# Kernel optimization log

Measured on AMD Instinct MI355X. Metric: run time of the kernel, lower is better.

Reference implementation:

```python
import jax, jax.numpy as jnp
import numpy as np

N_NODES = 50000
N_EDGES = 800000
F_IN = 64
HID = 256
EMB = 128
N_LAYERS = 3


def setup_inputs() -> dict:
    key = jax.random.key(0)
    ks = jax.random.split(key, 20)
    s = lambda i, shape: jax.random.normal(ks[i], shape, dtype=jnp.float32) * 0.05
    inp = {
        'x': jax.random.normal(ks[0], (N_NODES, F_IN), dtype=jnp.float32),
        'edge_index': jax.random.randint(ks[1], (2, N_EDGES), 0, N_NODES, dtype=jnp.int64),
        # node_encoder: Linear(F_IN,HID) -> ReLU -> Dropout -> Linear(HID,HID)
        'W1': s(2, (F_IN, HID)), 'b1': s(3, (HID,)),
        'W2': s(4, (HID, HID)), 'b2': s(5, (HID,)),
        # stacked GCN layer weights [L,HID,HID], biases [L,HID]
        'conv_W': s(6, (N_LAYERS, HID, HID)), 'conv_b': s(7, (N_LAYERS, HID)),
        # graph_projection: Linear(2H,H) -> ReLU -> Dropout -> Linear(H,EMB)
        'Wg1': s(8, (2 * HID, HID)), 'bg1': s(9, (HID,)),
        'Wg2': s(10, (HID, EMB)), 'bg2': s(11, (EMB,)),
        # decoder node_projection: Linear(EMB,H) -> ReLU -> Linear(H,H)
        'Wd1': s(12, (EMB, HID)), 'bd1': s(13, (HID,)),
        'Wd2': s(14, (HID, HID)), 'bd2': s(15, (HID,)),
    }
    return inp


def _forward(x, edge_index, W1, b1, W2, b2, conv_W, conv_b, Wg1, bg1, Wg2, bg2, Wd1, bd1, Wd2, bd2):
    N = x.shape[0]
    # node encoder (dropout is identity in eval)
    h = jax.nn.relu(x @ W1 + b1) @ W2 + b2  # [N,H]

    # GCN normalization with self-loops (PyG GCNConv defaults)
    self_idx = jnp.arange(N, dtype=edge_index.dtype)
    src = jnp.concatenate([edge_index[0], self_idx])  # [E+N]
    dst = jnp.concatenate([edge_index[1], self_idx])
    deg = jax.ops.segment_sum(jnp.ones_like(dst, dtype=h.dtype), dst, num_segments=N)
    dinv = jnp.where(deg > 0, jax.lax.rsqrt(deg), 0.0)
    norm = (dinv[src] * dinv[dst])[:, None]  # [E+N,1]

    for l in range(N_LAYERS):
        hw = h @ conv_W[l]                              # [N,H]
        msg = hw[src] * norm                            # gather + scale
        h = jax.ops.segment_sum(msg, dst, num_segments=N) + conv_b[l]
        h = jax.nn.relu(h)

    # global mean + max pool (single graph)
    graph_rep = jnp.concatenate([h.mean(axis=0), h.max(axis=0)])[None, :]  # [1,2H]
    graph_embedding = jax.nn.relu(graph_rep @ Wg1 + bg1) @ Wg2 + bg2       # [1,EMB]

    # decoder: project graph embedding, broadcast to all nodes, score edges
    v = jax.nn.relu(graph_embedding @ Wd1 + bd1) @ Wd2 + bd2  # [1,H]
    node_emb = jnp.broadcast_to(v, (N, v.shape[1]))           # [N,H]
    row, col = edge_index[0], edge_index[1]
    edge_logits = jnp.sum(node_emb[row] * node_emb[col], axis=1)  # [E]
    edge_probs = jax.nn.sigmoid(edge_logits)
    return graph_embedding, edge_probs


def reference(x, edge_index, W1, b1, W2, b2, conv_W, conv_b, Wg1, bg1, Wg2, bg2, Wd1, bd1, Wd2, bd2):
    return _forward(x, edge_index, W1, b1, W2, b2, conv_W, conv_b, Wg1, bg1, Wg2, bg2, Wd1, bd1, Wd2, bd2)
```

## Files before the change

### kernel.cpp

```cpp
#include <hip/hip_runtime.h>
#include <hip/hip_bf16.h>


typedef __attribute__((ext_vector_type(8))) short bf16x8;
typedef __attribute__((ext_vector_type(4))) float f32x4;
typedef __attribute__((ext_vector_type(2))) float f32x2;

#define FP8_SCALE 32.0f
#define FP8_INV (1.0f / 32.0f)

__device__ __forceinline__ ushort f2bf(float f) {
  union { float f; unsigned u; } v; v.f = f;
  unsigned r = v.u + 0x7FFF + ((v.u >> 16) & 1);
  return (ushort)(r >> 16);
}
__device__ __forceinline__ float bf2f(ushort b) {
  union { unsigned u; float f; } v; v.u = ((unsigned)b) << 16;
  return v.f;
}


__global__ void init_detect_kernel(const int* __restrict__ ei, int* __restrict__ flag,
                                   int* __restrict__ cnt8, int N8) {
  int i = blockIdx.x * 256 + threadIdx.x;
  if (i < N8) cnt8[i] = 0;
  if (blockIdx.x == 0 && threadIdx.x == 0) {
    int all0 = 1;
    for (int k = 0; k < 128; ++k) {
      if (ei[2 * k + 1] != 0) { all0 = 0; break; }
    }
    flag[0] = all0;
  }
}

__global__ void count_kernel(const int* __restrict__ ei, const int* __restrict__ flag,
                             int* __restrict__ cnt8, int* __restrict__ rank,
                             unsigned* __restrict__ pairs, int E, int N) {
  int e = blockIdx.x * 256 + threadIdx.x;
  if (e >= E) return;
  int s, d;
  if (flag[0]) {
    const long long* e64 = (const long long*)ei;
    s = (int)e64[e];
    d = (int)e64[(size_t)E + e];
  } else {
    s = ei[e];
    d = ei[(size_t)E + e];
  }
  rank[e] = atomicAdd(&cnt8[(size_t)(blockIdx.x & 7) * N + d], 1);
  pairs[e] = (unsigned)s | ((unsigned)d << 16);
}


__global__ __launch_bounds__(256) void bsum_kernel(const int* __restrict__ cnt8,
                                                   int* __restrict__ cnt,
                                                   int* __restrict__ bsum, int N) {
  __shared__ int red[4];
  int t = threadIdx.x;
  int i = blockIdx.x * 256 + t;
  int v = 0;
  if (i < N) {
#pragma unroll
    for (int c = 0; c < 8; ++c) v += cnt8[(size_t)c * N + i];
    cnt[i] = v;
  }
  for (int off = 32; off > 0; off >>= 1) v += __shfl_down(v, off, 64);
  if ((t & 63) == 0) red[t >> 6] = v;
  __syncthreads();
  if (t == 0) bsum[blockIdx.x] = red[0] + red[1] + red[2] + red[3];
}

__global__ __launch_bounds__(256) void bscan_kernel(const int* __restrict__ bsum,
                                                    int* __restrict__ boff,
                                                    int* __restrict__ rowptr, int B, int N) {
  __shared__ int s[256];
  int t = threadIdx.x;
  int v = (t < B) ? bsum[t] : 0;
  s[t] = v;
  __syncthreads();
  for (int off = 1; off < 256; off <<= 1) {
    int x = s[t];
    int add = (t >= off) ? s[t - off] : 0;
    __syncthreads();
    s[t] = x + add;
    __syncthreads();
  }
  if (t < B) boff[t] = s[t] - v;
  if (t == 255) rowptr[N] = s[255];
}

__global__ __launch_bounds__(256) void rowptr_kernel(const int* __restrict__ cnt,
                                                     const int* __restrict__ cnt8,
                                                     const int* __restrict__ boff,
                                                     int* __restrict__ rowptr,
                                                     int* __restrict__ base8,
                                                     float* __restrict__ dinv, int N) {
  __shared__ int s[256];
  int t = threadIdx.x;
  int i = blockIdx.x * 256 + t;
  int v = (i < N) ? cnt[i] : 0;
  s[t] = v;
  __syncthreads();
  for (int off = 1; off < 256; off <<= 1) {
    int x = s[t];
    int add = (t >= off) ? s[t - off] : 0;
    __syncthreads();
    s[t] = x + add;
    __syncthreads();
  }
  if (i < N) {
    int rp = boff[blockIdx.x] + s[t] - v;
    rowptr[i] = rp;
    int run = rp;
#pragma unroll
    for (int c = 0; c < 8; ++c) {
      base8[(size_t)c * N + i] = run;
      run += cnt8[(size_t)c * N + i];
    }
    dinv[i] = rsqrtf((float)(v + 1));
  }
}


__global__ void scatter_pack_kernel(const unsigned* __restrict__ pairs,
                                    const int* __restrict__ rank,
                                    const int* __restrict__ base8,
                                    ushort* __restrict__ col, int E, int N, int nScat,
                                    const float* __restrict__ W1, ushort* __restrict__ Wp1,
                                    const float* __restrict__ W2, ushort* __restrict__ Wp2,
                                    const float* __restrict__ cW, ushort* __restrict__ Wpc) {
  int b = blockIdx.x;
  if (b < nScat) {
    int e = b * 256 + threadIdx.x;
    if (e >= E) return;
    unsigned p = pairs[e];
    int s = p & 0xffff;
    int d = p >> 16;
    int c = (e >> 8) & 7;
    int pos = base8[(size_t)c * N + d] + rank[e];
    col[pos] = (ushort)s;
    return;
  }
  b -= nScat;
  const float* W;
  ushort* Wp;
  int K;
  if (b < 8) { W = W1; Wp = Wp1; K = 64; }
  else if (b < 40) { W = W2; Wp = Wp2; K = 256; b -= 8; }
  else {
    int l = (b - 40) >> 5;
    W = cW + (size_t)l * 256 * 256;
    Wp = Wpc + (size_t)l * 8 * 16 * 64 * 8;
    K = 256;
    b -= 40 + l * 32;
  }
  int idx = b * 256 + threadIdx.x;
  int total = (K >> 5) * 16 * 64;
  if (idx >= total) return;
  int lane = idx & 63;
  int cb = (idx >> 6) & 15;
  int ks = idx >> 10;
  int nn = cb * 16 + (lane & 15);
  int kbase = ks * 32 + (lane >> 4) * 8;
#pragma unroll
  for (int i = 0; i < 8; ++i)
    Wp[(size_t)idx * 8 + i] = f2bf(W[(size_t)(kbase + i) * 256 + nn]);
}


template <int NKS, bool AF32>
__global__ __launch_bounds__(256) void gemm_mfma_kernel(
    const void* __restrict__ Av,
    const ushort* __restrict__ Wp,
    const float* __restrict__ bias,
    const float* __restrict__ scale,
    ushort* __restrict__ C,
    unsigned char* __restrict__ C8,
    int M, int relu) {
  constexpr int K = NKS * 32;
  int t = threadIdx.x;
  int lane = t & 63, wave = t >> 6;
  int l15 = lane & 15, lk = lane >> 4;
  int row0 = blockIdx.x * 64;

  f32x4 acc[4][4];
#pragma unroll
  for (int rb = 0; rb < 4; ++rb)
#pragma unroll
    for (int cb = 0; cb < 4; ++cb) acc[rb][cb] = (f32x4){0.f, 0.f, 0.f, 0.f};

  const ushort* abase[4];
  const float* afbase[4];
#pragma unroll
  for (int rb = 0; rb < 4; ++rb) {
    int arow = row0 + rb * 16 + l15;
    if (AF32) arow = min(arow, M - 1);
    if (AF32) afbase[rb] = (const float*)Av + (size_t)arow * K + lk * 8;
    else      abase[rb] = (const ushort*)Av + (size_t)arow * K + lk * 8;
  }
  const ushort* bbase = Wp + ((size_t)(wave * 4) * 64 + lane) * 8;

#pragma unroll
  for (int ks = 0; ks < NKS; ++ks) {
    bf16x8 a[4], b[4];
#pragma unroll
    for (int rb = 0; rb < 4; ++rb) {
      if (AF32) {
        float4 f0 = *reinterpret_cast<const float4*>(afbase[rb] + ks * 32);
        float4 f1 = *reinterpret_cast<const float4*>(afbase[rb] + ks * 32 + 4);
        bf16x8 av;
        av[0] = (short)f2bf(f0.x); av[1] = (short)f2bf(f0.y);
        av[2] = (short)f2bf(f0.z); av[3] = (short)f2bf(f0.w);
        av[4] = (short)f2bf(f1.x); av[5] = (short)f2bf(f1.y);
        av[6] = (short)f2bf(f1.z); av[7] = (short)f2bf(f1.w);
        a[rb] = av;
      } else {
        a[rb] = *reinterpret_cast<const bf16x8*>(abase[rb] + ks * 32);
      }
    }
#pragma unroll
    for (int cb = 0; cb < 4; ++cb)
      b[cb] = *reinterpret_cast<const bf16x8*>(bbase + ((size_t)ks * 16 + cb) * 64 * 8);
#pragma unroll
    for (int rb = 0; rb < 4; ++rb)
#pragma unroll
      for (int cb = 0; cb < 4; ++cb)
        acc[rb][cb] = __builtin_amdgcn_mfma_f32_16x16x32_bf16(a[rb], b[cb], acc[rb][cb], 0, 0, 0);
  }

  float bv[4];
#pragma unroll
  for (int cb = 0; cb < 4; ++cb)
    bv[cb] = bias ? bias[wave * 64 + cb * 16 + l15] : 0.f;

#pragma unroll
  for (int rb = 0; rb < 4; ++rb) {
    int rbase = row0 + rb * 16 + lk * 4;
#pragma unroll
    for (int r = 0; r < 4; ++r) {
      int row = rbase + r;
      if (row >= M) continue;
      float sc = scale ? scale[row] : 1.f;
#pragma unroll
      for (int cb = 0; cb < 4; ++cb) {
        float v = acc[rb][cb][r] + bv[cb];
        if (relu) v = fmaxf(v, 0.f);
        v *= sc;
        int colIdx = wave * 64 + cb * 16 + l15;
        if (C8) {
          float vq = fminf(fmaxf(v * FP8_SCALE, -448.f), 448.f);
          unsigned p = __builtin_amdgcn_cvt_pk_fp8_f32(vq, vq, 0, false);
          C8[(size_t)row * 256 + colIdx] = (unsigned char)(p & 0xff);
        } else {
          C[(size_t)row * 256 + colIdx] = f2bf(v);
        }
      }
    }
  }
}


__global__ __launch_bounds__(64) void mp_kernel(const unsigned char* __restrict__ hw8,
                                                const int* __restrict__ rowptr,
                                                const ushort* __restrict__ col,
                                                const float* __restrict__ dinv,
                                                const float* __restrict__ bias,
                                                ushort* __restrict__ hout) {
  int n = blockIdx.x;
  int t = threadIdx.x;
  const unsigned* hw32 = reinterpret_cast<const unsigned*>(hw8);
  unsigned ws = hw32[(size_t)n * 64 + t];
  f32x2 lo = __builtin_amdgcn_cvt_pk_f32_fp8(ws, false);
  f32x2 hi = __builtin_amdgcn_cvt_pk_f32_fp8(ws, true);
  float ax = lo[0], ay = lo[1], az = hi[0], aw = hi[1];
  int beg = rowptr[n], end = rowptr[n + 1];
  int j = beg;
  for (; j + 16 <= end; j += 16) {
    int ss[16];
    unsigned ww[16];
#pragma unroll
    for (int q = 0; q < 16; ++q) ss[q] = col[j + q];
#pragma unroll
    for (int q = 0; q < 16; ++q) ww[q] = hw32[(size_t)ss[q] * 64 + t];
#pragma unroll
    for (int q = 0; q < 16; ++q) {
      f32x2 lq = __builtin_amdgcn_cvt_pk_f32_fp8(ww[q], false);
      f32x2 hq = __builtin_amdgcn_cvt_pk_f32_fp8(ww[q], true);
      ax += lq[0]; ay += lq[1]; az += hq[0]; aw += hq[1];
    }
  }
  for (; j + 4 <= end; j += 4) {
    int s0 = col[j], s1 = col[j + 1], s2 = col[j + 2], s3 = col[j + 3];
    unsigned w0 = hw32[(size_t)s0 * 64 + t];
    unsigned w1 = hw32[(size_t)s1 * 64 + t];
    unsigned w2 = hw32[(size_t)s2 * 64 + t];
    unsigned w3 = hw32[(size_t)s3 * 64 + t];
    f32x2 l0 = __builtin_amdgcn_cvt_pk_f32_fp8(w0, false);
    f32x2 h0 = __builtin_amdgcn_cvt_pk_f32_fp8(w0, true);
    f32x2 l1 = __builtin_amdgcn_cvt_pk_f32_fp8(w1, false);
    f32x2 h1 = __builtin_amdgcn_cvt_pk_f32_fp8(w1, true);
    f32x2 l2 = __builtin_amdgcn_cvt_pk_f32_fp8(w2, false);
    f32x2 h2 = __builtin_amdgcn_cvt_pk_f32_fp8(w2, true);
    f32x2 l3 = __builtin_amdgcn_cvt_pk_f32_fp8(w3, false);
    f32x2 h3 = __builtin_amdgcn_cvt_pk_f32_fp8(w3, true);
    ax += (l0[0] + l1[0]) + (l2[0] + l3[0]);
    ay += (l0[1] + l1[1]) + (l2[1] + l3[1]);
    az += (h0[0] + h1[0]) + (h2[0] + h3[0]);
    aw += (h0[1] + h1[1]) + (h2[1] + h3[1]);
  }
  for (; j < end; ++j) {
    int s = col[j];
    unsigned wv = hw32[(size_t)s * 64 + t];
    f32x2 l2 = __builtin_amdgcn_cvt_pk_f32_fp8(wv, false);
    f32x2 h2 = __builtin_amdgcn_cvt_pk_f32_fp8(wv, true);
    ax += l2[0]; ay += l2[1]; az += h2[0]; aw += h2[1];
  }
  float dn = dinv[n] * FP8_INV;
  float4 bv = *reinterpret_cast<const float4*>(bias + t * 4);
  ushort4 o;
  o.x = f2bf(fmaxf(fmaf(dn, ax, bv.x), 0.f));
  o.y = f2bf(fmaxf(fmaf(dn, ay, bv.y), 0.f));
  o.z = f2bf(fmaxf(fmaf(dn, az, bv.z), 0.f));
  o.w = f2bf(fmaxf(fmaf(dn, aw, bv.w), 0.f));
  *reinterpret_cast<ushort4*>(hout + (size_t)n * 256 + t * 4) = o;
}


__global__ __launch_bounds__(256) void pool_partial_kernel(const ushort* __restrict__ h,
                                                           float* __restrict__ psum,
                                                           float* __restrict__ pmax, int N) {
  __shared__ float ssum[4][256];
  __shared__ float smax[4][256];
  int t = threadIdx.x;
  int w = t >> 6, l = t & 63;
  int gw = blockIdx.x * 4 + w;
  float s0 = 0.f, s1 = 0.f, s2 = 0.f, s3 = 0.f;
  float m0 = 0.f, m1 = 0.f, m2 = 0.f, m3 = 0.f;
  const ushort4 z = {0, 0, 0, 0};
  for (int r = gw; r < N; r += 8192) {
    ushort4 v[8];
#pragma unroll
    for (int j = 0; j < 8; ++j) {
      int rj = r + j * 1024;
      v[j] = (rj < N) ? *reinterpret_cast<const ushort4*>(h + (size_t)rj * 256 + l * 4) : z;
    }
#pragma unroll
    for (int j = 0; j < 8; ++j) {
      float a0 = bf2f(v[j].x), a1 = bf2f(v[j].y), a2 = bf2f(v[j].z), a3 = bf2f(v[j].w);
      s0 += a0; s1 += a1; s2 += a2; s3 += a3;
      m0 = fmaxf(m0, a0); m1 = fmaxf(m1, a1); m2 = fmaxf(m2, a2); m3 = fmaxf(m3, a3);
    }
  }
  ssum[w][l * 4] = s0; ssum[w][l * 4 + 1] = s1; ssum[w][l * 4 + 2] = s2; ssum[w][l * 4 + 3] = s3;
  smax[w][l * 4] = m0; smax[w][l * 4 + 1] = m1; smax[w][l * 4 + 2] = m2; smax[w][l * 4 + 3] = m3;
  __syncthreads();
  float s = ssum[0][t] + ssum[1][t] + ssum[2][t] + ssum[3][t];
  float m = fmaxf(fmaxf(smax[0][t], smax[1][t]), fmaxf(smax[2][t], smax[3][t]));
  psum[(size_t)blockIdx.x * 256 + t] = s;
  pmax[(size_t)blockIdx.x * 256 + t] = m;
}


__global__ __launch_bounds__(1024) void head_kernel(const float* __restrict__ psum,
                                                    const float* __restrict__ pmax,
                                                    const float* __restrict__ Wg1, const float* __restrict__ bg1,
                                                    const float* __restrict__ Wg2, const float* __restrict__ bg2,
                                                    const float* __restrict__ Wd1, const float* __restrict__ bd1,
                                                    const float* __restrict__ Wd2, const float* __restrict__ bd2,
                                                    float* __restrict__ out_ge, float* __restrict__ s_out, int N) {
  __shared__ float gr[512];
  __shared__ float part[4][256];
  __shared__ float t1[256];
  __shared__ float ge[128];
  __shared__ float t2[256];
  __shared__ float vv[256];
  __shared__ float red[4];
  int t = threadIdx.x;
  float* pf = &part[0][0];

  {
    int kg = t >> 8, c = t & 255;
    const float* base = psum + (size_t)(kg * 64) * 256 + c;
    float a = 0.f;
#pragma unroll
    for (int i = 0; i < 64; i += 4)
      a += (base[(size_t)i * 256] + base[(size_t)(i + 1) * 256]) +
           (base[(size_t)(i + 2) * 256] + base[(size_t)(i + 3) * 256]);
    part[kg][c] = a;
  }
  __syncthreads();
  if (t < 256) gr[t] = (part[0][t] + part[1][t] + part[2][t] + part[3][t]) / (float)N;
  __syncthreads();
  {
    int kg = t >> 8, c = t & 255;
    const float* base = pmax + (size_t)(kg * 64) * 256 + c;
    float m = 0.f;
#pragma unroll
    for (int i = 0; i < 64; i += 4)
      m = fmaxf(m, fmaxf(fmaxf(base[(size_t)i * 256], base[(size_t)(i + 1) * 256]),
                         fmaxf(base[(size_t)(i + 2) * 256], base[(size_t)(i + 3) * 256])));
    part[kg][c] = m;
  }
  __syncthreads();
  if (t < 256)
    gr[256 + t] = fmaxf(fmaxf(part[0][t], part[1][t]), fmaxf(part[2][t], part[3][t]));
  __syncthreads();

  {
    int kg = t >> 8, c = t & 255, k0 = kg * 128;
    float a0 = 0, a1 = 0, a2 = 0, a3 = 0, a4 = 0, a5 = 0, a6 = 0, a7 = 0;
    for (int k = k0; k < k0 + 128; k += 8) {
      a0 = fmaf(gr[k + 0], Wg1[(size_t)(k + 0) * 256 + c], a0);
      a1 = fmaf(gr[k + 1], Wg1[(size_t)(k + 1) * 256 + c], a1);
      a2 = fmaf(gr[k + 2], Wg1[(size_t)(k + 2) * 256 + c], a2);
      a3 = fmaf(gr[k + 3], Wg1[(size_t)(k + 3) * 256 + c], a3);
      a4 = fmaf(gr[k + 4], Wg1[(size_t)(k + 4) * 256 + c], a4);
      a5 = fmaf(gr[k + 5], Wg1[(size_t)(k + 5) * 256 + c], a5);
      a6 = fmaf(gr[k + 6], Wg1[(size_t)(k + 6) * 256 + c], a6);
      a7 = fmaf(gr[k + 7], Wg1[(size_t)(k + 7) * 256 + c], a7);
    }
    part[kg][c] = ((a0 + a1) + (a2 + a3)) + ((a4 + a5) + (a6 + a7));
  }
  __syncthreads();
  if (t < 256) t1[t] = fmaxf(part[0][t] + part[1][t] + part[2][t] + part[3][t] + bg1[t], 0.f);
  __syncthreads();

  {
    int kg = t >> 7, c = t & 127, k0 = kg * 32;
    float a0 = 0, a1 = 0, a2 = 0, a3 = 0;
    for (int k = k0; k < k0 + 32; k += 4) {
      a0 = fmaf(t1[k + 0], Wg2[(size_t)(k + 0) * 128 + c], a0);
      a1 = fmaf(t1[k + 1], Wg2[(size_t)(k + 1) * 128 + c], a1);
      a2 = fmaf(t1[k + 2], Wg2[(size_t)(k + 2) * 128 + c], a2);
      a3 = fmaf(t1[k + 3], Wg2[(size_t)(k + 3) * 128 + c], a3);
    }
    pf[kg * 128 + c] = (a0 + a1) + (a2 + a3);
  }
  __syncthreads();
  if (t < 128) {
    float s = bg2[t];
#pragma unroll
    for (int g = 0; g < 8; ++g) s += pf[g * 128 + t];
    ge[t] = s;
    out_ge[t] = s;
  }
  __syncthreads();

  {
    int kg = t >> 8, c = t & 255, k0 = kg * 32;
    float a0 = 0, a1 = 0, a2 = 0, a3 = 0;
    for (int k = k0; k < k0 + 32; k += 4) {
      a0 = fmaf(ge[k + 0], Wd1[(size_t)(k + 0) * 256 + c], a0);
      a1 = fmaf(ge[k + 1], Wd1[(size_t)(k + 1) * 256 + c], a1);
      a2 = fmaf(ge[k + 2], Wd1[(size_t)(k + 2) * 256 + c], a2);
      a3 = fmaf(ge[k + 3], Wd1[(size_t)(k + 3) * 256 + c], a3);
    }
    part[kg][c] = (a0 + a1) + (a2 + a3);
  }
  __syncthreads();
  if (t < 256) t2[t] = fmaxf(part[0][t] + part[1][t] + part[2][t] + part[3][t] + bd1[t], 0.f);
  __syncthreads();

  {
    int kg = t >> 8, c = t & 255, k0 = kg * 64;
    float a0 = 0, a1 = 0, a2 = 0, a3 = 0, a4 = 0, a5 = 0, a6 = 0, a7 = 0;
    for (int k = k0; k < k0 + 64; k += 8) {
      a0 = fmaf(t2[k + 0], Wd2[(size_t)(k + 0) * 256 + c], a0);
      a1 = fmaf(t2[k + 1], Wd2[(size_t)(k + 1) * 256 + c], a1);
      a2 = fmaf(t2[k + 2], Wd2[(size_t)(k + 2) * 256 + c], a2);
      a3 = fmaf(t2[k + 3], Wd2[(size_t)(k + 3) * 256 + c], a3);
      a4 = fmaf(t2[k + 4], Wd2[(size_t)(k + 4) * 256 + c], a4);
      a5 = fmaf(t2[k + 5], Wd2[(size_t)(k + 5) * 256 + c], a5);
      a6 = fmaf(t2[k + 6], Wd2[(size_t)(k + 6) * 256 + c], a6);
      a7 = fmaf(t2[k + 7], Wd2[(size_t)(k + 7) * 256 + c], a7);
    }
    part[kg][c] = ((a0 + a1) + (a2 + a3)) + ((a4 + a5) + (a6 + a7));
  }
  __syncthreads();
  if (t < 256) vv[t] = part[0][t] + part[1][t] + part[2][t] + part[3][t] + bd2[t];
  __syncthreads();

  if (t < 256) {
    float p = vv[t] * vv[t];
    for (int off = 32; off > 0; off >>= 1) p += __shfl_down(p, off, 64);
    if ((t & 63) == 0) red[t >> 6] = p;
  }
  __syncthreads();
  if (t == 0) {
    float ssq = red[0] + red[1] + red[2] + red[3];
    s_out[0] = 1.f / (1.f + expf(-ssq));
  }
}

__global__ void fill_kernel(float* __restrict__ out, const float* __restrict__ s_out, int E) {
  int i = (blockIdx.x * 256 + threadIdx.x) * 4;
  if (i + 4 <= E) {
    float s = s_out[0];
    *reinterpret_cast<float4*>(out + i) = make_float4(s, s, s, s);
  } else {
    for (int j = i; j < E; ++j) out[j] = s_out[0];
  }
}


extern "C" void kernel_launch(void* const* d_in, const int* in_sizes, int n_in,
                              void* d_out, int out_size, void* d_ws, size_t ws_size,
                              hipStream_t stream) {
  const float* x   = (const float*)d_in[0];
  const int*   ei  = (const int*)d_in[1];
  const float* W1  = (const float*)d_in[2];
  const float* b1  = (const float*)d_in[3];
  const float* W2  = (const float*)d_in[4];
  const float* b2  = (const float*)d_in[5];
  const float* cW  = (const float*)d_in[6];
  const float* cb  = (const float*)d_in[7];
  const float* Wg1 = (const float*)d_in[8];
  const float* bg1 = (const float*)d_in[9];
  const float* Wg2 = (const float*)d_in[10];
  const float* bg2 = (const float*)d_in[11];
  const float* Wd1 = (const float*)d_in[12];
  const float* bd1 = (const float*)d_in[13];
  const float* Wd2 = (const float*)d_in[14];
  const float* bd2 = (const float*)d_in[15];
  float* out = (float*)d_out;

  int N = in_sizes[0] / 64;
  int E = in_sizes[1] / 2;
  int Mpad = (N + 63) & ~63;
  int B = (N + 255) / 256;

  size_t off = 0;
  auto walloc = [&](size_t bytes) -> void* {
    void* p = (char*)d_ws + off;
    off += (bytes + 511) & ~(size_t)511;
    return p;
  };
  ushort* hA    = (ushort*)walloc((size_t)Mpad * 256 * 2);
  ushort* hB    = (ushort*)walloc((size_t)Mpad * 256 * 2);
  unsigned char* hA8 = (unsigned char*)walloc((size_t)Mpad * 256);
  ushort* Wp1   = (ushort*)walloc((size_t)2 * 16 * 64 * 8 * 2);
  ushort* Wp2   = (ushort*)walloc((size_t)8 * 16 * 64 * 8 * 2);
  ushort* Wpc   = (ushort*)walloc((size_t)3 * 8 * 16 * 64 * 8 * 2);
  int*   cnt8   = (int*)walloc((size_t)8 * N * 4);
  int*   cnt    = (int*)walloc((size_t)N * 4);
  int*   rowptr = (int*)walloc(((size_t)N + 1) * 4);
  int*   base8  = (int*)walloc((size_t)8 * N * 4);
  int*   rank   = (int*)walloc((size_t)E * 4);
  unsigned* pairs = (unsigned*)walloc((size_t)E * 4);
  float* dinv   = (float*)walloc((size_t)N * 4);
  ushort* col   = (ushort*)walloc((size_t)E * 2);
  int*   bsum   = (int*)walloc(256 * 4);
  int*   boff   = (int*)walloc(256 * 4);
  float* psum   = (float*)walloc((size_t)256 * 256 * 4);
  float* pmax   = (float*)walloc((size_t)256 * 256 * 4);
  float* s_out  = (float*)walloc(512);
  int*   flag   = (int*)walloc(512);

  init_detect_kernel<<<(8 * N + 255) / 256, 256, 0, stream>>>(ei, flag, cnt8, 8 * N);
  count_kernel<<<(E + 255) / 256, 256, 0, stream>>>(ei, flag, cnt8, rank, pairs, E, N);
  bsum_kernel<<<B, 256, 0, stream>>>(cnt8, cnt, bsum, N);
  bscan_kernel<<<1, 256, 0, stream>>>(bsum, boff, rowptr, B, N);
  rowptr_kernel<<<B, 256, 0, stream>>>(cnt, cnt8, boff, rowptr, base8, dinv, N);
  int nScat = (E + 255) / 256;
  scatter_pack_kernel<<<nScat + 8 + 32 + 96, 256, 0, stream>>>(
      pairs, rank, base8, col, E, N, nScat, W1, Wp1, W2, Wp2, cW, Wpc);

  int gblocks = Mpad / 64;
  gemm_mfma_kernel<2, true><<<gblocks, 256, 0, stream>>>(x, Wp1, b1, nullptr, hA, nullptr, N, 1);
  gemm_mfma_kernel<8, false><<<gblocks, 256, 0, stream>>>(hA, Wp2, b2, nullptr, hB, nullptr, N, 0);
  for (int l = 0; l < 3; ++l) {
    gemm_mfma_kernel<8, false><<<gblocks, 256, 0, stream>>>(
        hB, Wpc + (size_t)l * 8 * 16 * 64 * 8, nullptr, dinv, nullptr, hA8, N, 0);
    mp_kernel<<<N, 64, 0, stream>>>(hA8, rowptr, col, dinv, cb + (size_t)l * 256, hB);
  }
  pool_partial_kernel<<<256, 256, 0, stream>>>(hB, psum, pmax, N);
  head_kernel<<<1, 1024, 0, stream>>>(psum, pmax, Wg1, bg1, Wg2, bg2, Wd1, bd1, Wd2, bd2,
                                      out, s_out, N);
  fill_kernel<<<(E + 1023) / 1024, 256, 0, stream>>>(out + 128, s_out, E);
}
```

Before: 346.5 us.

## Split message passing into feature chunks with 16 nodes per block

Replaces the one-node-per-64-thread-block aggregation with a 256-thread kernel where each block handles 16 nodes over one 64-byte feature chunk. Consecutive blocks cover nodes for the same chunk, which narrows the gather working set to a quarter of the fp8 feature matrix at a time and is meant to improve cache hit rates for random neighbor gathers. The inner unroll drops from 16 to 8 and the 4-wide tail loop is removed. The trade-off is that each 16-lane group now loads only 64 bytes per neighbor and re-reads the column indices four times, once per chunk.

```diff
diff --git a/kernel.cpp b/kernel.cpp
--- a/kernel.cpp
+++ b/kernel.cpp
@@ -260,69 +260,59 @@
 }
 
 
-__global__ __launch_bounds__(64) void mp_kernel(const unsigned char* __restrict__ hw8,
-                                                const int* __restrict__ rowptr,
-                                                const ushort* __restrict__ col,
-                                                const float* __restrict__ dinv,
-                                                const float* __restrict__ bias,
-                                                ushort* __restrict__ hout) {
-  int n = blockIdx.x;
-  int t = threadIdx.x;
+__global__ __launch_bounds__(256) void mp_chunk_kernel(const unsigned char* __restrict__ hw8,
+                                                       const int* __restrict__ rowptr,
+                                                       const ushort* __restrict__ col,
+                                                       const float* __restrict__ dinv,
+                                                       const float* __restrict__ bias,
+                                                       ushort* __restrict__ hout,
+                                                       int N, int bpc) {
+  int chunk = blockIdx.x / bpc;
+  int nb = blockIdx.x - chunk * bpc;
+  int t = threadIdx.x;
+  int g = t >> 4;
+  int l = t & 15;
+  int n = nb * 16 + g;
+  if (n >= N) return;
+  int cd = chunk * 16 + l;
   const unsigned* hw32 = reinterpret_cast<const unsigned*>(hw8);
-  unsigned ws = hw32[(size_t)n * 64 + t];
+
+  unsigned ws = hw32[(size_t)n * 64 + cd];
   f32x2 lo = __builtin_amdgcn_cvt_pk_f32_fp8(ws, false);
   f32x2 hi = __builtin_amdgcn_cvt_pk_f32_fp8(ws, true);
   float ax = lo[0], ay = lo[1], az = hi[0], aw = hi[1];
+
   int beg = rowptr[n], end = rowptr[n + 1];
   int j = beg;
-  for (; j + 16 <= end; j += 16) {
-    int ss[16];
-    unsigned ww[16];
-#pragma unroll
-    for (int q = 0; q < 16; ++q) ss[q] = col[j + q];
-#pragma unroll
-    for (int q = 0; q < 16; ++q) ww[q] = hw32[(size_t)ss[q] * 64 + t];
-#pragma unroll
-    for (int q = 0; q < 16; ++q) {
+  for (; j + 8 <= end; j += 8) {
+    int ss[8];
+    unsigned ww[8];
+#pragma unroll
+    for (int q = 0; q < 8; ++q) ss[q] = col[j + q];
+#pragma unroll
+    for (int q = 0; q < 8; ++q) ww[q] = hw32[(size_t)ss[q] * 64 + cd];
+#pragma unroll
+    for (int q = 0; q < 8; ++q) {
       f32x2 lq = __builtin_amdgcn_cvt_pk_f32_fp8(ww[q], false);
       f32x2 hq = __builtin_amdgcn_cvt_pk_f32_fp8(ww[q], true);
       ax += lq[0]; ay += lq[1]; az += hq[0]; aw += hq[1];
     }
   }
-  for (; j + 4 <= end; j += 4) {
-    int s0 = col[j], s1 = col[j + 1], s2 = col[j + 2], s3 = col[j + 3];
-    unsigned w0 = hw32[(size_t)s0 * 64 + t];
-    unsigned w1 = hw32[(size_t)s1 * 64 + t];
-    unsigned w2 = hw32[(size_t)s2 * 64 + t];
-    unsigned w3 = hw32[(size_t)s3 * 64 + t];
-    f32x2 l0 = __builtin_amdgcn_cvt_pk_f32_fp8(w0, false);
-    f32x2 h0 = __builtin_amdgcn_cvt_pk_f32_fp8(w0, true);
-    f32x2 l1 = __builtin_amdgcn_cvt_pk_f32_fp8(w1, false);
-    f32x2 h1 = __builtin_amdgcn_cvt_pk_f32_fp8(w1, true);
-    f32x2 l2 = __builtin_amdgcn_cvt_pk_f32_fp8(w2, false);
-    f32x2 h2 = __builtin_amdgcn_cvt_pk_f32_fp8(w2, true);
-    f32x2 l3 = __builtin_amdgcn_cvt_pk_f32_fp8(w3, false);
-    f32x2 h3 = __builtin_amdgcn_cvt_pk_f32_fp8(w3, true);
-    ax += (l0[0] + l1[0]) + (l2[0] + l3[0]);
-    ay += (l0[1] + l1[1]) + (l2[1] + l3[1]);
-    az += (h0[0] + h1[0]) + (h2[0] + h3[0]);
-    aw += (h0[1] + h1[1]) + (h2[1] + h3[1]);
-  }
   for (; j < end; ++j) {
     int s = col[j];
-    unsigned wv = hw32[(size_t)s * 64 + t];
+    unsigned wv = hw32[(size_t)s * 64 + cd];
     f32x2 l2 = __builtin_amdgcn_cvt_pk_f32_fp8(wv, false);
     f32x2 h2 = __builtin_amdgcn_cvt_pk_f32_fp8(wv, true);
     ax += l2[0]; ay += l2[1]; az += h2[0]; aw += h2[1];
   }
   float dn = dinv[n] * FP8_INV;
-  float4 bv = *reinterpret_cast<const float4*>(bias + t * 4);
+  float4 bv = *reinterpret_cast<const float4*>(bias + cd * 4);
   ushort4 o;
   o.x = f2bf(fmaxf(fmaf(dn, ax, bv.x), 0.f));
   o.y = f2bf(fmaxf(fmaf(dn, ay, bv.y), 0.f));
   o.z = f2bf(fmaxf(fmaf(dn, az, bv.z), 0.f));
   o.w = f2bf(fmaxf(fmaf(dn, aw, bv.w), 0.f));
-  *reinterpret_cast<ushort4*>(hout + (size_t)n * 256 + t * 4) = o;
+  *reinterpret_cast<ushort4*>(hout + (size_t)n * 256 + cd * 4) = o;
 }
 
 
@@ -568,10 +558,12 @@
   int gblocks = Mpad / 64;
   gemm_mfma_kernel<2, true><<<gblocks, 256, 0, stream>>>(x, Wp1, b1, nullptr, hA, nullptr, N, 1);
   gemm_mfma_kernel<8, false><<<gblocks, 256, 0, stream>>>(hA, Wp2, b2, nullptr, hB, nullptr, N, 0);
+  int bpc = (N + 15) / 16;
   for (int l = 0; l < 3; ++l) {
     gemm_mfma_kernel<8, false><<<gblocks, 256, 0, stream>>>(
         hB, Wpc + (size_t)l * 8 * 16 * 64 * 8, nullptr, dinv, nullptr, hA8, N, 0);
-    mp_kernel<<<N, 64, 0, stream>>>(hA8, rowptr, col, dinv, cb + (size_t)l * 256, hB);
+    mp_chunk_kernel<<<4 * bpc, 256, 0, stream>>>(hA8, rowptr, col, dinv,
+                                                 cb + (size_t)l * 256, hB, N, bpc);
   }
   pool_partial_kernel<<<256, 256, 0, stream>>>(hB, psum, pmax, N);
   head_kernel<<<1, 1024, 0, stream>>>(psum, pmax, Wg1, bg1, Wg2, bg2, Wd1, bd1, Wd2, bd2,
```

New measurement: 408.9 us. +18.0%, slower.
